# Kernel optimization log

Hardware: AMD Instinct MI355X
Metric: run time of the kernel (lower is better)

Reference implementation:

```python
import jax, jax.numpy as jnp
import numpy as np

K = 4
C = 512
CLAMP = (1e-4, 1.0 - 1e-4)
INIT_ALPHAS = (0.8, 0.9, 0.98, 0.99)


def setup_inputs() -> dict:
    key = jax.random.key(0)
    kx, = jax.random.split(key, 1)
    B, T = 16, 4096
    x = jax.random.normal(kx, (B, T, C), dtype=jnp.float32)
    # logit_alpha: [K, C], each row initialized to logit(alpha_k)
    alphas = np.clip(np.array(INIT_ALPHAS[:K], dtype=np.float32), CLAMP[0], CLAMP[1])
    logit = np.log(alphas / (1.0 - alphas))  # logit
    logit_alpha = jnp.asarray(np.repeat(logit[:, None], C, axis=1), dtype=jnp.float32)
    mix_logits = jnp.zeros((C, K), dtype=jnp.float32)
    return {"x": x, "logit_alpha": logit_alpha, "mix_logits": mix_logits}


def reference(x, logit_alpha, mix_logits):
    # x: [B, T, C]; logit_alpha: [K, C]; mix_logits: [C, K]
    B, T, Cc = x.shape
    x32 = x.astype(jnp.float32)
    a = jnp.clip(jax.nn.sigmoid(logit_alpha.astype(jnp.float32)), CLAMP[0], CLAMP[1])  # [K, C]
    one_minus_a = 1.0 - a

    y0 = jnp.broadcast_to(x32[:, 0, None, :], (B, K, Cc))  # [B, K, C]

    def step(y_prev, xt):  # y_prev: [B,K,C], xt: [B,C]
        y = a * y_prev + one_minus_a * xt[:, None, :]
        return y, y

    xs = jnp.swapaxes(x32[:, 1:, :], 0, 1)  # [T-1, B, C]
    _, ys = jax.lax.scan(step, y0, xs)  # ys: [T-1, B, K, C]
    yk_all = jnp.concatenate([y0[None], ys], axis=0)  # [T, B, K, C]

    mix = jax.nn.softmax(mix_logits.astype(jnp.float32), axis=-1)  # [C, K]
    trend = jnp.einsum('tbkc,ck->btc', yk_all, mix)
    return trend.astype(x.dtype)
```

## Files before the change

kernel.cpp:

```cpp
#include <hip/hip_runtime.h>

#define B_  16
#define T_  4096
#define C_  512
#define K_  4
#define NT_ 64
#define L_  (T_ / NT_)

__device__ __forceinline__ float sigmoid_clamp(float la) {
    float av = 1.0f / (1.0f + expf(-la));
    return fminf(fmaxf(av, 1e-4f), 1.0f - 1e-4f);
}

__global__ __launch_bounds__(512) void ema_pass1(const float* __restrict__ x,
                                                 const float* __restrict__ logit_alpha,
                                                 float* __restrict__ ws) {
    const int c = threadIdx.x;
    const int b = blockIdx.x / NT_;
    const int j = blockIdx.x % NT_;

    float a[K_], oma[K_], s[K_];
#pragma unroll
    for (int k = 0; k < K_; ++k) {
        float av = sigmoid_clamp(logit_alpha[k * C_ + c]);
        a[k] = av; oma[k] = 1.0f - av; s[k] = 0.0f;
    }

    const float* xp = x + ((size_t)b * T_ + (size_t)j * L_) * C_ + c;
#pragma unroll 4
    for (int i = 0; i < L_; ++i) {
        float xv = xp[(size_t)i * C_];
#pragma unroll
        for (int k = 0; k < K_; ++k)
            s[k] = fmaf(a[k], s[k], oma[k] * xv);
    }

#pragma unroll
    for (int k = 0; k < K_; ++k)
        ws[(((size_t)b * K_ + k) * NT_ + j) * C_ + c] = s[k];
}

__global__ __launch_bounds__(512) void ema_pass2(const float* __restrict__ x,
                                                 const float* __restrict__ logit_alpha,
                                                 float* __restrict__ ws) {
    const int c = threadIdx.x;
    const int b = blockIdx.x / K_;
    const int k = blockIdx.x % K_;

    float av = sigmoid_clamp(logit_alpha[k * C_ + c]);
    float A = av;
#pragma unroll
    for (int q = 0; q < 6; ++q) A *= A;

    float carry = x[(size_t)b * T_ * C_ + c];
    float* wsb = ws + ((size_t)b * K_ + k) * NT_ * C_ + c;
    for (int j = 0; j < NT_; ++j) {
        float sj = wsb[(size_t)j * C_];
        wsb[(size_t)j * C_] = carry;
        carry = fmaf(A, carry, sj);
    }
}

__global__ __launch_bounds__(512) void ema_pass3(const float* __restrict__ x,
                                                 const float* __restrict__ logit_alpha,
                                                 const float* __restrict__ mix_logits,
                                                 const float* __restrict__ ws,
                                                 float* __restrict__ out) {
    const int c = threadIdx.x;
    const int b = blockIdx.x / NT_;
    const int j = blockIdx.x % NT_;

    float a[K_], oma[K_], y[K_], m[K_];
#pragma unroll
    for (int k = 0; k < K_; ++k) {
        float av = sigmoid_clamp(logit_alpha[k * C_ + c]);
        a[k] = av; oma[k] = 1.0f - av;
        y[k] = ws[(((size_t)b * K_ + k) * NT_ + j) * C_ + c];
    }

    float mx = -INFINITY;
#pragma unroll
    for (int k = 0; k < K_; ++k) { m[k] = mix_logits[(size_t)c * K_ + k]; mx = fmaxf(mx, m[k]); }
    float den = 0.0f;
#pragma unroll
    for (int k = 0; k < K_; ++k) { m[k] = expf(m[k] - mx); den += m[k]; }
    float inv = 1.0f / den;
#pragma unroll
    for (int k = 0; k < K_; ++k) m[k] *= inv;

    const float* xp = x + ((size_t)b * T_ + (size_t)j * L_) * C_ + c;
    float*       op = out + ((size_t)b * T_ + (size_t)j * L_) * C_ + c;
#pragma unroll 4
    for (int i = 0; i < L_; ++i) {
        float xv = xp[(size_t)i * C_];
        float acc = 0.0f;
#pragma unroll
        for (int k = 0; k < K_; ++k) {
            y[k] = fmaf(a[k], y[k], oma[k] * xv);
            acc = fmaf(m[k], y[k], acc);
        }
        op[(size_t)i * C_] = acc;
    }
}

extern "C" void kernel_launch(void* const* d_in, const int* in_sizes, int n_in,
                              void* d_out, int out_size, void* d_ws, size_t ws_size,
                              hipStream_t stream) {
    const float* x           = (const float*)d_in[0];
    const float* logit_alpha = (const float*)d_in[1];
    const float* mix_logits  = (const float*)d_in[2];
    float* out = (float*)d_out;
    float* ws  = (float*)d_ws;

    ema_pass1<<<B_ * NT_, 512, 0, stream>>>(x, logit_alpha, ws);
    ema_pass2<<<B_ * K_,  512, 0, stream>>>(x, logit_alpha, ws);
    ema_pass3<<<B_ * NT_, 512, 0, stream>>>(x, logit_alpha, mix_logits, ws, out);
}
```

Before: 72.98 us.

## Fuse three-pass EMA scan into single chunked kernel with in-block parallel prefix

Replaces the three kernels (chunk reduce, carry scan, replay) with one fused kernel. Each block owns one batch row and 32 channels and walks time in 512-step chunks. Within a chunk it combines a per-thread serial scan, a wave shuffle prefix and a cross-wave LDS prefix using precomputed powers of alpha. It also uses float4 vector loads, nontemporal loads and stores, and prefetches the next chunk. This reads x once instead of twice and drops the workspace round trip. In exchange it launches only 256 blocks and adds a barrier per chunk, which may limit occupancy and latency hiding.

```diff
diff --git a/kernel.cpp b/kernel.cpp
--- a/kernel.cpp
+++ b/kernel.cpp
@@ -4,102 +4,192 @@
 #define T_  4096
 #define C_  512
 #define K_  4
-#define NT_ 64
-#define L_  (T_ / NT_)
+#define C4_ (C_ / 4)
+
+#define NW_     8
+#define SUBW_   8
+#define NSUB_   (NW_ * SUBW_)
+#define LSUB_   8
+#define CHUNK_  (NSUB_ * LSUB_)
+#define NCHUNK_ (T_ / CHUNK_)
+#define CT_     32
+#define NCT_    (C_ / CT_)
+
+typedef float f4 __attribute__((ext_vector_type(4)));
 
 __device__ __forceinline__ float sigmoid_clamp(float la) {
     float av = 1.0f / (1.0f + expf(-la));
     return fminf(fmaxf(av, 1e-4f), 1.0f - 1e-4f);
 }
 
-__global__ __launch_bounds__(512) void ema_pass1(const float* __restrict__ x,
-                                                 const float* __restrict__ logit_alpha,
-                                                 float* __restrict__ ws) {
-    const int c = threadIdx.x;
-    const int b = blockIdx.x / NT_;
-    const int j = blockIdx.x % NT_;
-
-    float a[K_], oma[K_], s[K_];
+__device__ __forceinline__ f4 shflup4(f4 v, int delta) {
+    f4 r;
+    r.x = __shfl_up(v.x, delta, 64);
+    r.y = __shfl_up(v.y, delta, 64);
+    r.z = __shfl_up(v.z, delta, 64);
+    r.w = __shfl_up(v.w, delta, 64);
+    return r;
+}
+
+__global__ __launch_bounds__(512, 2) void ema_fused(
+    const f4* __restrict__ x4,
+    const float* __restrict__ logit_alpha,
+    const f4* __restrict__ ml4,
+    f4* __restrict__ out4)
+{
+    __shared__ f4 POW8[9][K_][8];
+    __shared__ f4 POW64[9][K_][8];
+    __shared__ f4 WT[2][NW_][K_][8];
+
+    const int tid  = threadIdx.x;
+    const int wv   = tid >> 6;
+    const int lane = tid & 63;
+    const int subl = lane >> 3;
+    const int c4l  = lane & 7;
+    const int sub  = (wv << 3) | subl;
+
+    const int b  = blockIdx.x >> 4;
+    const int ct = blockIdx.x & 15;
+    const int c4 = ct * 8 + c4l;
+
+    f4 one = {1.f, 1.f, 1.f, 1.f};
+    f4 zero = {0.f, 0.f, 0.f, 0.f};
+    f4 a[K_], oma[K_], m[K_];
 #pragma unroll
     for (int k = 0; k < K_; ++k) {
-        float av = sigmoid_clamp(logit_alpha[k * C_ + c]);
-        a[k] = av; oma[k] = 1.0f - av; s[k] = 0.0f;
-    }
-
-    const float* xp = x + ((size_t)b * T_ + (size_t)j * L_) * C_ + c;
-#pragma unroll 4
-    for (int i = 0; i < L_; ++i) {
-        float xv = xp[(size_t)i * C_];
+        f4 la = ((const f4*)logit_alpha)[k * C4_ + c4];
+        f4 av;
+        av.x = sigmoid_clamp(la.x); av.y = sigmoid_clamp(la.y);
+        av.z = sigmoid_clamp(la.z); av.w = sigmoid_clamp(la.w);
+        a[k] = av; oma[k] = one - av;
+    }
+#pragma unroll
+    for (int ci = 0; ci < 4; ++ci) {
+        f4 ml = ml4[c4 * 4 + ci];
+        float mx = fmaxf(fmaxf(ml.x, ml.y), fmaxf(ml.z, ml.w));
+        float e0 = expf(ml.x - mx), e1 = expf(ml.y - mx);
+        float e2 = expf(ml.z - mx), e3 = expf(ml.w - mx);
+        float inv = 1.0f / (e0 + e1 + e2 + e3);
+        m[0][ci] = e0 * inv; m[1][ci] = e1 * inv;
+        m[2][ci] = e2 * inv; m[3][ci] = e3 * inv;
+    }
+
+    if (tid < 32) {
+        const int kk = tid >> 3, cc = tid & 7;
+        f4 av = a[kk];
+        f4 A8 = av * av; A8 = A8 * A8; A8 = A8 * A8;
+        f4 cur = one;
+        POW8[0][kk][cc] = cur;
+#pragma unroll
+        for (int s = 1; s <= 8; ++s) { cur = cur * A8; POW8[s][kk][cc] = cur; }
+        f4 A64 = cur;
+        cur = one;
+        POW64[0][kk][cc] = cur;
+#pragma unroll
+        for (int w = 1; w <= 8; ++w) { cur = cur * A64; POW64[w][kk][cc] = cur; }
+    }
+    __syncthreads();
+
+    const size_t basein = (size_t)b * T_ * C4_ + c4;
+    f4 x0 = x4[basein];
+    f4 Asub[K_], Gw[K_];
+#pragma unroll
+    for (int k = 0; k < K_; ++k) {
+        Asub[k] = POW8[subl][k][c4l];
+        Gw[k]   = POW64[wv][k][c4l] * x0;
+    }
+
+    const int trow = sub * LSUB_;
+    f4 xc[LSUB_];
+#pragma unroll
+    for (int i = 0; i < LSUB_; ++i)
+        xc[i] = __builtin_nontemporal_load(&x4[basein + (size_t)(trow + i) * C4_]);
+
+#pragma unroll 1
+    for (int ch = 0; ch < NCHUNK_; ++ch) {
+        f4 xn[LSUB_];
+        if (ch + 1 < NCHUNK_) {
+#pragma unroll
+            for (int i = 0; i < LSUB_; ++i)
+                xn[i] = __builtin_nontemporal_load(
+                    &x4[basein + (size_t)((ch + 1) * CHUNK_ + trow + i) * C4_]);
+        }
+
+        f4 s[K_];
+#pragma unroll
+        for (int k = 0; k < K_; ++k) s[k] = zero;
+#pragma unroll
+        for (int i = 0; i < LSUB_; ++i) {
+            f4 xv = xc[i];
+#pragma unroll
+            for (int k = 0; k < K_; ++k) s[k] = a[k] * s[k] + oma[k] * xv;
+        }
+
+#pragma unroll
+        for (int st = 0; st < 3; ++st) {
+            const int dd = 1 << st;
+#pragma unroll
+            for (int k = 0; k < K_; ++k) {
+                f4 Mv = POW8[dd][k][c4l];
+                f4 r  = shflup4(s[k], dd * 8);
+                f4 t2 = s[k] + Mv * r;
+                s[k] = (subl >= dd) ? t2 : s[k];
+            }
+        }
+        f4 Ils[K_];
+#pragma unroll
+        for (int k = 0; k < K_; ++k) {
+            f4 r = shflup4(s[k], 8);
+            Ils[k] = (subl >= 1) ? r : zero;
+        }
+
+        const int pb = ch & 1;
+        if (subl == 7) {
+#pragma unroll
+            for (int k = 0; k < K_; ++k) WT[pb][wv][k][c4l] = s[k];
+        }
+        asm volatile("s_waitcnt lgkmcnt(0)" ::: "memory");
+        __builtin_amdgcn_s_barrier();
+
+        f4 P[K_], acc[K_], A64r[K_];
+#pragma unroll
+        for (int k = 0; k < K_; ++k) {
+            P[k] = zero; acc[k] = zero; A64r[k] = POW64[1][k][c4l];
+        }
+#pragma unroll
+        for (int w = 0; w < NW_; ++w) {
+#pragma unroll
+            for (int k = 0; k < K_; ++k) {
+                if (w == wv) P[k] = acc[k];
+                acc[k] = A64r[k] * acc[k] + WT[pb][w][k][c4l];
+            }
+        }
+
+        f4 y[K_];
+#pragma unroll
+        for (int k = 0; k < K_; ++k) y[k] = Asub[k] * (Gw[k] + P[k]) + Ils[k];
+
+        const size_t ob = basein + (size_t)(ch * CHUNK_ + trow) * C4_;
+#pragma unroll
+        for (int i = 0; i < LSUB_; ++i) {
+            f4 xv = xc[i];
+            f4 o = zero;
+#pragma unroll
+            for (int k = 0; k < K_; ++k) {
+                y[k] = a[k] * y[k] + oma[k] * xv;
+                o = o + m[k] * y[k];
+            }
+            __builtin_nontemporal_store(o, &out4[ob + (size_t)i * C4_]);
+        }
+
 #pragma unroll
         for (int k = 0; k < K_; ++k)
-            s[k] = fmaf(a[k], s[k], oma[k] * xv);
-    }
-
-#pragma unroll
-    for (int k = 0; k < K_; ++k)
-        ws[(((size_t)b * K_ + k) * NT_ + j) * C_ + c] = s[k];
-}
-
-__global__ __launch_bounds__(512) void ema_pass2(const float* __restrict__ x,
-                                                 const float* __restrict__ logit_alpha,
-                                                 float* __restrict__ ws) {
-    const int c = threadIdx.x;
-    const int b = blockIdx.x / K_;
-    const int k = blockIdx.x % K_;
-
-    float av = sigmoid_clamp(logit_alpha[k * C_ + c]);
-    float A = av;
-#pragma unroll
-    for (int q = 0; q < 6; ++q) A *= A;
-
-    float carry = x[(size_t)b * T_ * C_ + c];
-    float* wsb = ws + ((size_t)b * K_ + k) * NT_ * C_ + c;
-    for (int j = 0; j < NT_; ++j) {
-        float sj = wsb[(size_t)j * C_];
-        wsb[(size_t)j * C_] = carry;
-        carry = fmaf(A, carry, sj);
-    }
-}
-
-__global__ __launch_bounds__(512) void ema_pass3(const float* __restrict__ x,
-                                                 const float* __restrict__ logit_alpha,
-                                                 const float* __restrict__ mix_logits,
-                                                 const float* __restrict__ ws,
-                                                 float* __restrict__ out) {
-    const int c = threadIdx.x;
-    const int b = blockIdx.x / NT_;
-    const int j = blockIdx.x % NT_;
-
-    float a[K_], oma[K_], y[K_], m[K_];
-#pragma unroll
-    for (int k = 0; k < K_; ++k) {
-        float av = sigmoid_clamp(logit_alpha[k * C_ + c]);
-        a[k] = av; oma[k] = 1.0f - av;
-        y[k] = ws[(((size_t)b * K_ + k) * NT_ + j) * C_ + c];
-    }
-
-    float mx = -INFINITY;
-#pragma unroll
-    for (int k = 0; k < K_; ++k) { m[k] = mix_logits[(size_t)c * K_ + k]; mx = fmaxf(mx, m[k]); }
-    float den = 0.0f;
-#pragma unroll
-    for (int k = 0; k < K_; ++k) { m[k] = expf(m[k] - mx); den += m[k]; }
-    float inv = 1.0f / den;
-#pragma unroll
-    for (int k = 0; k < K_; ++k) m[k] *= inv;
-
-    const float* xp = x + ((size_t)b * T_ + (size_t)j * L_) * C_ + c;
-    float*       op = out + ((size_t)b * T_ + (size_t)j * L_) * C_ + c;
-#pragma unroll 4
-    for (int i = 0; i < L_; ++i) {
-        float xv = xp[(size_t)i * C_];
-        float acc = 0.0f;
-#pragma unroll
-        for (int k = 0; k < K_; ++k) {
-            y[k] = fmaf(a[k], y[k], oma[k] * xv);
-            acc = fmaf(m[k], y[k], acc);
-        }
-        op[(size_t)i * C_] = acc;
+            Gw[k] = POW64[NW_][k][c4l] * Gw[k] + POW64[wv][k][c4l] * acc[k];
+
+        if (ch + 1 < NCHUNK_) {
+#pragma unroll
+            for (int i = 0; i < LSUB_; ++i) xc[i] = xn[i];
+        }
     }
 }
 
@@ -110,9 +200,7 @@
     const float* logit_alpha = (const float*)d_in[1];
     const float* mix_logits  = (const float*)d_in[2];
     float* out = (float*)d_out;
-    float* ws  = (float*)d_ws;
-
-    ema_pass1<<<B_ * NT_, 512, 0, stream>>>(x, logit_alpha, ws);
-    ema_pass2<<<B_ * K_,  512, 0, stream>>>(x, logit_alpha, ws);
-    ema_pass3<<<B_ * NT_, 512, 0, stream>>>(x, logit_alpha, mix_logits, ws, out);
-}
+
+    ema_fused<<<B_ * NCT_, 512, 0, stream>>>((const f4*)x, logit_alpha,
+                                             (const f4*)mix_logits, (f4*)out);
+}
```

New measurement: 105.4 us. 1.44x slower.
